# Performance work log

Measured on AMD Instinct MI355X. Metric: run time of the kernel, lower is better.

## Reference

```python
import jax, jax.numpy as jnp
import numpy as np

NEG_INF = -1e9


def sparsemax(e):
    # e: (B, T); sparsemax along last dim (Martins & Astudillo 2016)
    z = e - jnp.max(e, axis=-1, keepdims=True)
    zs = jnp.sort(z, axis=-1)[..., ::-1]                       # descending
    T = z.shape[-1]
    r = jnp.arange(1, T + 1, dtype=z.dtype)                    # (T,)
    bound = 1.0 + r * zs
    cs = jnp.cumsum(zs, axis=-1)
    is_gt = (bound > cs).astype(z.dtype)
    k = jnp.max(is_gt * r, axis=-1, keepdims=True)
    tau = (jnp.sum(is_gt * zs, axis=-1, keepdims=True) - 1.0) / k
    return jnp.maximum(0.0, z - tau)


def setup_inputs() -> dict:
    key = jax.random.key(0)
    ks = jax.random.split(key, 8)
    B, T, D, H = 64, 4096, 256, 256
    scale = 1.0 / np.sqrt(D)
    inp = {
        "input": jax.random.normal(ks[0], (B, T, D), dtype=jnp.float32),
        "mask": jax.random.randint(ks[1], (B, T), 0, 2, dtype=jnp.int32),
        "Wq": jax.random.uniform(ks[2], (D, H), jnp.float32, -scale, scale),
        "bq": jnp.zeros((H,), jnp.float32),
        "Wk": jax.random.uniform(ks[3], (D, H), jnp.float32, -scale, scale),
        "bk": jnp.zeros((H,), jnp.float32),
        "Wv": jax.random.uniform(ks[4], (D, H), jnp.float32, -scale, scale),
        "bv": jnp.zeros((H,), jnp.float32),
        "rate": jnp.ones((T,), jnp.float32),
    }
    return inp


def reference(input, mask, Wq, bq, Wk, bk, Wv, bv, rate):
    # input: (B, T, D); mask: (B, T) int
    q = jnp.mean(input, axis=1) @ Wq + bq        # (B, H)  mean-pooled query
    k = input @ Wk + bk                          # (B, T, H)
    v = input @ Wv + bv                          # (B, T, H)
    e = jnp.einsum("bth,bh->bt", k, q)          # mul attention scores
    m = mask.astype(e.dtype)
    time_miss = jnp.log1p((1.0 - jax.nn.sigmoid(e)) * m)
    e = e - rate * time_miss                     # rate: (T,) broadcasts over B
    e = jnp.where(mask == 0, NEG_INF, e)
    a = sparsemax(e)                             # (B, T)
    out = jnp.einsum("bt,bth->bh", a, v)        # weighted sum -> (B, H)
    return (out, a)
```

## Files before the change

kernel.cpp:

```cpp
#include <hip/hip_runtime.h>
#include <math.h>

#define BB 64
#define TT 4096
#define DD 256
#define HH 256
#define NEG_INF_F (-1e9f)


__global__ __launch_bounds__(256) void k_colsum(const float* __restrict__ input,
                                                float* __restrict__ partials) {
    int chunk = blockIdx.x;
    int b = blockIdx.y;
    int tid = threadIdx.x;
    int tsub = tid >> 6;
    int d4 = tid & 63;
    const float4* base = (const float4*)(input + ((size_t)b * TT + (size_t)chunk * 128) * DD);
    float4 acc = make_float4(0.f, 0.f, 0.f, 0.f);
#pragma unroll 8
    for (int t = tsub; t < 128; t += 4) {
        float4 v = base[(size_t)t * 64 + d4];
        acc.x += v.x; acc.y += v.y; acc.z += v.z; acc.w += v.w;
    }
    __shared__ float4 sm[256];
    sm[tid] = acc;
    __syncthreads();
    if (tid < 64) {
        float4 a0 = sm[tid], a1 = sm[tid + 64], a2 = sm[tid + 128], a3 = sm[tid + 192];
        float4 r = make_float4(a0.x + a1.x + a2.x + a3.x,
                               a0.y + a1.y + a2.y + a3.y,
                               a0.z + a1.z + a2.z + a3.z,
                               a0.w + a1.w + a2.w + a3.w);
        ((float4*)(partials + ((size_t)b * 32 + chunk) * 256))[tid] = r;
    }
}

__global__ __launch_bounds__(256) void k_small(const float* __restrict__ partials,
                                               const float* __restrict__ Wq,
                                               const float* __restrict__ bq,
                                               const float* __restrict__ Wk,
                                               const float* __restrict__ bk,
                                               float* __restrict__ wkq,
                                               float* __restrict__ ek) {
    int b = blockIdx.x, tid = threadIdx.x;
    int wave = tid >> 6, lane = tid & 63;
    __shared__ __align__(16) float mr[DD];
    __shared__ __align__(16) float qsh[HH];
    __shared__ float red[4];
    const float* pb = partials + (size_t)b * 32 * 256;
    float s = 0.f;
#pragma unroll
    for (int c = 0; c < 32; ++c) s += pb[c * 256 + tid];
    mr[tid] = s * (1.0f / (float)TT);
    __syncthreads();
    float acc = bq[tid];
#pragma unroll 8
    for (int d = 0; d < DD; ++d) acc += mr[d] * Wq[d * HH + tid];
    qsh[tid] = acc;
    float p = bk[tid] * acc;
#pragma unroll
    for (int off = 32; off > 0; off >>= 1) p += __shfl_down(p, off);
    if (lane == 0) red[wave] = p;
    __syncthreads();
    if (tid == 0) ek[b] = red[0] + red[1] + red[2] + red[3];
    float4 qv = ((const float4*)qsh)[lane];
    for (int i = 0; i < 64; ++i) {
        int d = wave * 64 + i;
        float4 wv = ((const float4*)(Wk + (size_t)d * HH))[lane];
        float t = wv.x * qv.x + wv.y * qv.y + wv.z * qv.z + wv.w * qv.w;
#pragma unroll
        for (int off = 32; off > 0; off >>= 1) t += __shfl_down(t, off);
        if (lane == 0) wkq[b * DD + d] = t;
    }
}

__global__ __launch_bounds__(256) void k_scores(const float* __restrict__ input,
                                                const float* __restrict__ wkq,
                                                const float* __restrict__ ek,
                                                const int* __restrict__ mask,
                                                const float* __restrict__ rate,
                                                float* __restrict__ e_out) {
    int job = (int)gridDim.x - 1 - (int)blockIdx.x;
    int b = job >> 4;
    int t0 = (job & 15) << 8;
    int tid = threadIdx.x;
    int wave = tid >> 6, lane = tid & 63;
    int g = lane >> 4, s = lane & 15;

    __shared__ __align__(16) float wsh[DD];
    __shared__ float esh[256];
    __shared__ int wbase[4];
    __shared__ short actlist[256];

    int m = mask[b * TT + t0 + tid];
    bool act = (m != 0);
    unsigned long long bal = __ballot(act);
    if (lane == 0) wbase[wave] = __popcll(bal);
    wsh[tid] = wkq[b * DD + tid];
    esh[tid] = NEG_INF_F;
    __syncthreads();
    int base = 0;
#pragma unroll
    for (int w = 0; w < 4; ++w) base += (w < wave) ? wbase[w] : 0;
    int nact = wbase[0] + wbase[1] + wbase[2] + wbase[3];
    int pos = base + __popcll(bal & ((1ull << lane) - 1ull));
    if (act) actlist[pos] = (short)tid;
    const float4* wsh4 = (const float4*)wsh;
    float4 w0 = wsh4[s], w1 = wsh4[16 + s], w2 = wsh4[32 + s], w3 = wsh4[48 + s];
    float ekb = ek[b];
    __syncthreads();

    const float4* rows = (const float4*)(input + ((size_t)b * TT + t0) * DD);
    for (int i0 = wave * 8; i0 < nact; i0 += 32) {
        int ia = i0 + g, ib = i0 + 4 + g;
        bool va = (ia < nact), vb = (ib < nact);
        int ra = va ? actlist[ia] : actlist[0];
        int rb = vb ? actlist[ib] : actlist[0];
        const float4* rpa = rows + (size_t)ra * 64 + s;
        const float4* rpb = rows + (size_t)rb * 64 + s;
        float4 a0 = rpa[0], a1 = rpa[16], a2 = rpa[32], a3 = rpa[48];
        float4 b0 = rpb[0], b1 = rpb[16], b2 = rpb[32], b3 = rpb[48];
        float pa = a0.x * w0.x + a0.y * w0.y + a0.z * w0.z + a0.w * w0.w
                 + a1.x * w1.x + a1.y * w1.y + a1.z * w1.z + a1.w * w1.w
                 + a2.x * w2.x + a2.y * w2.y + a2.z * w2.z + a2.w * w2.w
                 + a3.x * w3.x + a3.y * w3.y + a3.z * w3.z + a3.w * w3.w;
        float pb = b0.x * w0.x + b0.y * w0.y + b0.z * w0.z + b0.w * w0.w
                 + b1.x * w1.x + b1.y * w1.y + b1.z * w1.z + b1.w * w1.w
                 + b2.x * w2.x + b2.y * w2.y + b2.z * w2.z + b2.w * w2.w
                 + b3.x * w3.x + b3.y * w3.y + b3.z * w3.z + b3.w * w3.w;
#pragma unroll
        for (int off = 8; off > 0; off >>= 1) {
            pa += __shfl_down(pa, off, 16);
            pb += __shfl_down(pb, off, 16);
        }
        if (s == 0) {
            if (va) {
                float e0 = pa + ekb;
                float sg = 1.f / (1.f + expf(e0));
                esh[ra] = e0 - rate[t0 + ra] * log1pf(sg);
            }
            if (vb) {
                float e1 = pb + ekb;
                float sg = 1.f / (1.f + expf(e1));
                esh[rb] = e1 - rate[t0 + rb] * log1pf(sg);
            }
        }
    }
    __syncthreads();
    e_out[b * TT + t0 + tid] = esh[tid];
}

__global__ __launch_bounds__(1024) void k_fin(const float* __restrict__ e_in,
                                              const float* __restrict__ input,
                                              const float* __restrict__ Wv,
                                              const float* __restrict__ bv,
                                              float* __restrict__ out,
                                              float* __restrict__ a_out) {
    int b = blockIdx.x, tid = threadIdx.x;
    int wave = tid >> 6, lane = tid & 63;
    __shared__ float za[TT];
    __shared__ int s_supp[TT];
    __shared__ __align__(16) float part[16 * DD];
    __shared__ __align__(16) float s_sh[DD];
    __shared__ float redM[16];
    __shared__ float redS[2][16], redC[2][16];
    __shared__ int cnt;

    const float* er = e_in + (size_t)b * TT;
    float z0 = er[tid], z1 = er[tid + 1024], z2 = er[tid + 2048], z3 = er[tid + 3072];
    float lmax = fmaxf(fmaxf(z0, z1), fmaxf(z2, z3));
#pragma unroll
    for (int off = 32; off > 0; off >>= 1) lmax = fmaxf(lmax, __shfl_xor(lmax, off));
    if (lane == 0) redM[wave] = lmax;
    if (tid == 0) cnt = 0;
    __syncthreads();
    float mx = redM[0];
#pragma unroll
    for (int i = 1; i < 16; ++i) mx = fmaxf(mx, redM[i]);
    z0 = fmaxf(z0 - mx, -1.0f); z1 = fmaxf(z1 - mx, -1.0f);
    z2 = fmaxf(z2 - mx, -1.0f); z3 = fmaxf(z3 - mx, -1.0f);
    za[tid] = z0; za[tid + 1024] = z1; za[tid + 2048] = z2; za[tid + 3072] = z3;

    float tau = -1.0f;
    int prevc = -1;
    for (int it = 0; it < 32; ++it) {
        int pb = it & 1;
        float s = 0.f, c = 0.f;
        if (z0 > tau) { s += z0; c += 1.f; }
        if (z1 > tau) { s += z1; c += 1.f; }
        if (z2 > tau) { s += z2; c += 1.f; }
        if (z3 > tau) { s += z3; c += 1.f; }
#pragma unroll
        for (int off = 32; off > 0; off >>= 1) {
            s += __shfl_xor(s, off);
            c += __shfl_xor(c, off);
        }
        if (lane == 0) { redS[pb][wave] = s; redC[pb][wave] = c; }
        __syncthreads();
        float ss = 0.f, cc = 0.f;
#pragma unroll
        for (int i = 0; i < 16; ++i) { ss += redS[pb][i]; cc += redC[pb][i]; }
        tau = (ss - 1.f) / cc;
        int ci = (int)cc;
        if (ci == prevc) break;
        prevc = ci;
    }

    float a0 = fmaxf(z0 - tau, 0.f), a1 = fmaxf(z1 - tau, 0.f);
    float a2 = fmaxf(z2 - tau, 0.f), a3 = fmaxf(z3 - tau, 0.f);
    float* ar = a_out + (size_t)b * TT;
    ar[tid] = a0; ar[tid + 1024] = a1; ar[tid + 2048] = a2; ar[tid + 3072] = a3;
    if (a0 > 0.f) s_supp[atomicAdd(&cnt, 1)] = tid;
    if (a1 > 0.f) s_supp[atomicAdd(&cnt, 1)] = tid + 1024;
    if (a2 > 0.f) s_supp[atomicAdd(&cnt, 1)] = tid + 2048;
    if (a3 > 0.f) s_supp[atomicAdd(&cnt, 1)] = tid + 3072;
    float lsum = a0 + a1 + a2 + a3;
#pragma unroll
    for (int off = 32; off > 0; off >>= 1) lsum += __shfl_xor(lsum, off);
    if (lane == 0) redM[wave] = lsum;
    __syncthreads();
    float suma = 0.f;
#pragma unroll
    for (int i = 0; i < 16; ++i) suma += redM[i];

    float4 acc = make_float4(0.f, 0.f, 0.f, 0.f);
    int cl = cnt;
    for (int i = wave; i < cl; i += 16) {
        int t = s_supp[i];
        float av = fmaxf(za[t] - tau, 0.f);
        float4 v = ((const float4*)(input + ((size_t)b * TT + t) * DD))[lane];
        acc.x += av * v.x; acc.y += av * v.y; acc.z += av * v.z; acc.w += av * v.w;
    }
    ((float4*)part)[wave * 64 + lane] = acc;
    __syncthreads();
    if (tid < 256) {
        float s = 0.f;
#pragma unroll
        for (int w = 0; w < 16; ++w) s += part[w * 256 + tid];
        s_sh[tid] = s;
    }
    __syncthreads();
    int h = tid & 255;
    int g = tid >> 8;
    float o = 0.f;
#pragma unroll 8
    for (int d = g * 64; d < g * 64 + 64; ++d) o += s_sh[d] * Wv[(size_t)d * HH + h];
    part[g * 256 + h] = o;
    __syncthreads();
    if (tid < 256) {
        float o4 = part[tid] + part[256 + tid] + part[512 + tid] + part[768 + tid]
                 + suma * bv[tid];
        out[b * HH + tid] = o4;
    }
}

extern "C" void kernel_launch(void* const* d_in, const int* in_sizes, int n_in,
                              void* d_out, int out_size, void* d_ws, size_t ws_size,
                              hipStream_t stream) {
    const float* input = (const float*)d_in[0];
    const int*   mask  = (const int*)d_in[1];
    const float* Wq    = (const float*)d_in[2];
    const float* bq    = (const float*)d_in[3];
    const float* Wk    = (const float*)d_in[4];
    const float* bk    = (const float*)d_in[5];
    const float* Wv    = (const float*)d_in[6];
    const float* bv    = (const float*)d_in[7];
    const float* rate  = (const float*)d_in[8];

    float* out   = (float*)d_out;
    float* a_out = out + BB * HH;

    float* ws       = (float*)d_ws;
    float* partials = ws;
    float* wkq      = ws + 524288;
    float* ek       = ws + 540672;
    float* e        = ws + 540736;

    k_colsum<<<dim3(32, BB), 256, 0, stream>>>(input, partials);
    k_small<<<BB, 256, 0, stream>>>(partials, Wq, bq, Wk, bk, wkq, ek);
    k_scores<<<(BB * TT) / 256, 256, 0, stream>>>(input, wkq, ek, mask, rate, e);
    k_fin<<<BB, 1024, 0, stream>>>(e, input, Wv, bv, out, a_out);
}
```

Before: 127.3 us.

## Fuse query/Wk projection into score kernel and process four rows per iteration

Removes the k_small launch by having every k_scores block recompute the mean-pooled query, the bk·q bias term, and the Wk·q vector in shared memory. This saves one kernel launch and a global round trip for wkq/ek. In exchange, the 256x256 Wq and Wk matvecs are recomputed redundantly in all 16 blocks per batch, which adds L2 traffic and compute before the main loop. The scoring loop also now handles four active rows per 16-lane group per iteration instead of two, to expose more memory-level parallelism.

```diff
diff --git a/kernel.cpp b/kernel.cpp
--- a/kernel.cpp
+++ b/kernel.cpp
@@ -35,48 +35,12 @@
     }
 }
 
-__global__ __launch_bounds__(256) void k_small(const float* __restrict__ partials,
-                                               const float* __restrict__ Wq,
-                                               const float* __restrict__ bq,
-                                               const float* __restrict__ Wk,
-                                               const float* __restrict__ bk,
-                                               float* __restrict__ wkq,
-                                               float* __restrict__ ek) {
-    int b = blockIdx.x, tid = threadIdx.x;
-    int wave = tid >> 6, lane = tid & 63;
-    __shared__ __align__(16) float mr[DD];
-    __shared__ __align__(16) float qsh[HH];
-    __shared__ float red[4];
-    const float* pb = partials + (size_t)b * 32 * 256;
-    float s = 0.f;
-#pragma unroll
-    for (int c = 0; c < 32; ++c) s += pb[c * 256 + tid];
-    mr[tid] = s * (1.0f / (float)TT);
-    __syncthreads();
-    float acc = bq[tid];
-#pragma unroll 8
-    for (int d = 0; d < DD; ++d) acc += mr[d] * Wq[d * HH + tid];
-    qsh[tid] = acc;
-    float p = bk[tid] * acc;
-#pragma unroll
-    for (int off = 32; off > 0; off >>= 1) p += __shfl_down(p, off);
-    if (lane == 0) red[wave] = p;
-    __syncthreads();
-    if (tid == 0) ek[b] = red[0] + red[1] + red[2] + red[3];
-    float4 qv = ((const float4*)qsh)[lane];
-    for (int i = 0; i < 64; ++i) {
-        int d = wave * 64 + i;
-        float4 wv = ((const float4*)(Wk + (size_t)d * HH))[lane];
-        float t = wv.x * qv.x + wv.y * qv.y + wv.z * qv.z + wv.w * qv.w;
-#pragma unroll
-        for (int off = 32; off > 0; off >>= 1) t += __shfl_down(t, off);
-        if (lane == 0) wkq[b * DD + d] = t;
-    }
-}
-
 __global__ __launch_bounds__(256) void k_scores(const float* __restrict__ input,
-                                                const float* __restrict__ wkq,
-                                                const float* __restrict__ ek,
+                                                const float* __restrict__ partials,
+                                                const float* __restrict__ Wq,
+                                                const float* __restrict__ bq,
+                                                const float* __restrict__ Wk,
+                                                const float* __restrict__ bk,
                                                 const int* __restrict__ mask,
                                                 const float* __restrict__ rate,
                                                 float* __restrict__ e_out) {
@@ -87,8 +51,11 @@
     int wave = tid >> 6, lane = tid & 63;
     int g = lane >> 4, s = lane & 15;
 
+    __shared__ __align__(16) float mr[DD];
+    __shared__ __align__(16) float qsh[HH];
     __shared__ __align__(16) float wsh[DD];
     __shared__ float esh[256];
+    __shared__ float red[4];
     __shared__ int wbase[4];
     __shared__ short actlist[256];
 
@@ -96,7 +63,11 @@
     bool act = (m != 0);
     unsigned long long bal = __ballot(act);
     if (lane == 0) wbase[wave] = __popcll(bal);
-    wsh[tid] = wkq[b * DD + tid];
+    const float* pbp = partials + (size_t)b * 32 * 256;
+    float ssum = 0.f;
+#pragma unroll
+    for (int c = 0; c < 32; ++c) ssum += pbp[c * 256 + tid];
+    mr[tid] = ssum * (1.0f / (float)TT);
     esh[tid] = NEG_INF_F;
     __syncthreads();
     int base = 0;
@@ -105,21 +76,54 @@
     int nact = wbase[0] + wbase[1] + wbase[2] + wbase[3];
     int pos = base + __popcll(bal & ((1ull << lane) - 1ull));
     if (act) actlist[pos] = (short)tid;
+
+    float q = bq[tid];
+#pragma unroll 8
+    for (int d = 0; d < DD; ++d) q += mr[d] * Wq[d * HH + tid];
+    qsh[tid] = q;
+    float p = bk[tid] * q;
+#pragma unroll
+    for (int off = 32; off > 0; off >>= 1) p += __shfl_down(p, off);
+    if (lane == 0) red[wave] = p;
+    __syncthreads();
+    float ekb = red[0] + red[1] + red[2] + red[3];
+
+    const float4* q4 = (const float4*)qsh;
+    float4 q0 = q4[s], q1 = q4[16 + s], q2 = q4[32 + s], q3 = q4[48 + s];
+    int grp = wave * 4 + g;
+#pragma unroll 4
+    for (int j = 0; j < 16; ++j) {
+        int d = grp * 16 + j;
+        const float4* wk4 = (const float4*)(Wk + (size_t)d * HH);
+        float4 r0 = wk4[s], r1 = wk4[16 + s], r2 = wk4[32 + s], r3 = wk4[48 + s];
+        float t = r0.x * q0.x + r0.y * q0.y + r0.z * q0.z + r0.w * q0.w
+                + r1.x * q1.x + r1.y * q1.y + r1.z * q1.z + r1.w * q1.w
+                + r2.x * q2.x + r2.y * q2.y + r2.z * q2.z + r2.w * q2.w
+                + r3.x * q3.x + r3.y * q3.y + r3.z * q3.z + r3.w * q3.w;
+#pragma unroll
+        for (int off = 8; off > 0; off >>= 1) t += __shfl_down(t, off, 16);
+        if (s == 0) wsh[d] = t;
+    }
+    __syncthreads();
+
     const float4* wsh4 = (const float4*)wsh;
     float4 w0 = wsh4[s], w1 = wsh4[16 + s], w2 = wsh4[32 + s], w3 = wsh4[48 + s];
-    float ekb = ek[b];
-    __syncthreads();
-
     const float4* rows = (const float4*)(input + ((size_t)b * TT + t0) * DD);
-    for (int i0 = wave * 8; i0 < nact; i0 += 32) {
-        int ia = i0 + g, ib = i0 + 4 + g;
-        bool va = (ia < nact), vb = (ib < nact);
+    for (int i0 = wave * 16; i0 < nact; i0 += 64) {
+        int ia = i0 + g, ib = i0 + 4 + g, ic = i0 + 8 + g, id_ = i0 + 12 + g;
+        bool va = (ia < nact), vb = (ib < nact), vc = (ic < nact), vd = (id_ < nact);
         int ra = va ? actlist[ia] : actlist[0];
         int rb = vb ? actlist[ib] : actlist[0];
+        int rc = vc ? actlist[ic] : actlist[0];
+        int rd = vd ? actlist[id_] : actlist[0];
         const float4* rpa = rows + (size_t)ra * 64 + s;
         const float4* rpb = rows + (size_t)rb * 64 + s;
+        const float4* rpc = rows + (size_t)rc * 64 + s;
+        const float4* rpd = rows + (size_t)rd * 64 + s;
         float4 a0 = rpa[0], a1 = rpa[16], a2 = rpa[32], a3 = rpa[48];
         float4 b0 = rpb[0], b1 = rpb[16], b2 = rpb[32], b3 = rpb[48];
+        float4 c0 = rpc[0], c1 = rpc[16], c2 = rpc[32], c3 = rpc[48];
+        float4 d0 = rpd[0], d1 = rpd[16], d2 = rpd[32], d3 = rpd[48];
         float pa = a0.x * w0.x + a0.y * w0.y + a0.z * w0.z + a0.w * w0.w
                  + a1.x * w1.x + a1.y * w1.y + a1.z * w1.z + a1.w * w1.w
                  + a2.x * w2.x + a2.y * w2.y + a2.z * w2.z + a2.w * w2.w
@@ -128,22 +132,30 @@
                  + b1.x * w1.x + b1.y * w1.y + b1.z * w1.z + b1.w * w1.w
                  + b2.x * w2.x + b2.y * w2.y + b2.z * w2.z + b2.w * w2.w
                  + b3.x * w3.x + b3.y * w3.y + b3.z * w3.z + b3.w * w3.w;
+        float pc = c0.x * w0.x + c0.y * w0.y + c0.z * w0.z + c0.w * w0.w
+                 + c1.x * w1.x + c1.y * w1.y + c1.z * w1.z + c1.w * w1.w
+                 + c2.x * w2.x + c2.y * w2.y + c2.z * w2.z + c2.w * w2.w
+                 + c3.x * w3.x + c3.y * w3.y + c3.z * w3.z + c3.w * w3.w;
+        float pd = d0.x * w0.x + d0.y * w0.y + d0.z * w0.z + d0.w * w0.w
+                 + d1.x * w1.x + d1.y * w1.y + d1.z * w1.z + d1.w * w1.w
+                 + d2.x * w2.x + d2.y * w2.y + d2.z * w2.z + d2.w * w2.w
+                 + d3.x * w3.x + d3.y * w3.y + d3.z * w3.z + d3.w * w3.w;
 #pragma unroll
         for (int off = 8; off > 0; off >>= 1) {
             pa += __shfl_down(pa, off, 16);
             pb += __shfl_down(pb, off, 16);
+            pc += __shfl_down(pc, off, 16);
+            pd += __shfl_down(pd, off, 16);
         }
         if (s == 0) {
-            if (va) {
-                float e0 = pa + ekb;
-                float sg = 1.f / (1.f + expf(e0));
-                esh[ra] = e0 - rate[t0 + ra] * log1pf(sg);
-            }
-            if (vb) {
-                float e1 = pb + ekb;
-                float sg = 1.f / (1.f + expf(e1));
-                esh[rb] = e1 - rate[t0 + rb] * log1pf(sg);
-            }
+            if (va) { float e0 = pa + ekb; float sg = 1.f / (1.f + expf(e0));
+                      esh[ra] = e0 - rate[t0 + ra] * log1pf(sg); }
+            if (vb) { float e1 = pb + ekb; float sg = 1.f / (1.f + expf(e1));
+                      esh[rb] = e1 - rate[t0 + rb] * log1pf(sg); }
+            if (vc) { float e2 = pc + ekb; float sg = 1.f / (1.f + expf(e2));
+                      esh[rc] = e2 - rate[t0 + rc] * log1pf(sg); }
+            if (vd) { float e3 = pd + ekb; float sg = 1.f / (1.f + expf(e3));
+                      esh[rd] = e3 - rate[t0 + rd] * log1pf(sg); }
         }
     }
     __syncthreads();
@@ -272,12 +284,10 @@
 
     float* ws       = (float*)d_ws;
     float* partials = ws;
-    float* wkq      = ws + 524288;
-    float* ek       = ws + 540672;
-    float* e        = ws + 540736;
+    float* e        = ws + 524288;
 
     k_colsum<<<dim3(32, BB), 256, 0, stream>>>(input, partials);
-    k_small<<<BB, 256, 0, stream>>>(partials, Wq, bq, Wk, bk, wkq, ek);
-    k_scores<<<(BB * TT) / 256, 256, 0, stream>>>(input, wkq, ek, mask, rate, e);
+    k_scores<<<(BB * TT) / 256, 256, 0, stream>>>(input, partials, Wq, bq, Wk, bk,
+                                                  mask, rate, e);
     k_fin<<<BB, 1024, 0, stream>>>(e, input, Wv, bv, out, a_out);
 }
```

After: 108.0 us. -15.1%, faster.
